# Optimization experiments

Measured on AMD Instinct MI355X. Metric: run time of the kernel, lower is better.

The kernel has to match this reference:

```python
import jax, jax.numpy as jnp
import numpy as np

DIM = 4096

def _fwht_unnormalized(y):
    # y: (T, d), iterative radix-2 butterfly, unnormalized Sylvester WHT
    d = y.shape[-1]
    h = 1
    while h < d:
        y = y.reshape(-1, d // (2 * h), 2, h)
        a = y[..., 0, :]
        b = y[..., 1, :]
        y = jnp.stack([a + b, a - b], axis=-2).reshape(-1, d)
        h *= 2
    return y

def setup_inputs() -> dict:
    key = jax.random.key(0)
    x = jax.random.normal(key, (4, 2048, DIM), dtype=jnp.float32)
    return {"x": x}

def reference(x):
    # Original: x_flat @ H.T where H is built recursively with a 1/sqrt(n)
    # division at EVERY recursion level. H is symmetric, and equals the
    # unnormalized Sylvester Hadamard times 2^{-L(L+1)/4}, L = log2(d).
    shape = x.shape
    d = shape[-1]
    L = int(round(np.log2(d)))
    scale = np.float32(2.0 ** (-(L * (L + 1)) / 4.0))
    y = _fwht_unnormalized(x.reshape(-1, d))
    return (y * scale).reshape(shape)
```

## Files before the change

kernel.cpp:

```cpp
#include <hip/hip_runtime.h>


constexpr int DIM = 4096;
constexpr int PITCH = 68;

__global__ __launch_bounds__(64) void fwht4096_kernel(const float* __restrict__ x,
                                                      float* __restrict__ y) {
    __shared__ float buf[64 * PITCH];
    const int lane = threadIdx.x;
    const long long row = blockIdx.x;

    float v[64];

    {
        const float4* src = reinterpret_cast<const float4*>(x + row * DIM + lane * 64);
#pragma unroll
        for (int q = 0; q < 16; ++q) {
            float4 t = src[q];
            v[4 * q + 0] = t.x;
            v[4 * q + 1] = t.y;
            v[4 * q + 2] = t.z;
            v[4 * q + 3] = t.w;
        }
    }

#pragma unroll
    for (int h = 1; h < 64; h <<= 1) {
#pragma unroll
        for (int i = 0; i < 64; i += 2 * h) {
#pragma unroll
            for (int k = 0; k < h; ++k) {
                float a = v[i + k];
                float b = v[i + k + h];
                v[i + k]     = a + b;
                v[i + k + h] = a - b;
            }
        }
    }

    {
        float* wp = buf + lane * PITCH;
#pragma unroll
        for (int q = 0; q < 16; ++q) {
            float4 t;
            t.x = v[4 * q + 0];
            t.y = v[4 * q + 1];
            t.z = v[4 * q + 2];
            t.w = v[4 * q + 3];
            reinterpret_cast<float4*>(wp)[q] = t;
        }
    }
    __syncthreads();

#pragma unroll
    for (int m = 0; m < 64; ++m) {
        v[m] = buf[m * PITCH + lane];
    }

#pragma unroll
    for (int h = 1; h < 64; h <<= 1) {
#pragma unroll
        for (int i = 0; i < 64; i += 2 * h) {
#pragma unroll
            for (int k = 0; k < h; ++k) {
                float a = v[i + k];
                float b = v[i + k + h];
                v[i + k]     = a + b;
                v[i + k + h] = a - b;
            }
        }
    }

    const float scale = 0x1p-39f;
    float* dst = y + row * DIM + lane;
#pragma unroll
    for (int m = 0; m < 64; ++m) {
        dst[m * 64] = v[m] * scale;
    }
}

extern "C" void kernel_launch(void* const* d_in, const int* in_sizes, int n_in,
                              void* d_out, int out_size, void* d_ws, size_t ws_size,
                              hipStream_t stream) {
    const float* x = (const float*)d_in[0];
    float* y = (float*)d_out;
    const int nrows = in_sizes[0] / DIM;
    fwht4096_kernel<<<nrows, 64, 0, stream>>>(x, y);
}
```

Measured before the change: 229.1 us.

## Split 4096-point FWHT into three radix-16 stages across 256 threads

Restructures the per-row transform from two radix-64 passes over 64 threads into three radix-16 passes over 256 threads, with two shared-memory transposes padded to 17 floats per row. Each thread now holds 16 values instead of 64, which cuts register pressure and raises occupancy and latency hiding for a memory-bound kernel. In exchange it adds an extra LDS round trip and more block barriers per row.

```diff
diff --git a/kernel.cpp b/kernel.cpp
--- a/kernel.cpp
+++ b/kernel.cpp
@@ -2,32 +2,12 @@
 
 
 constexpr int DIM = 4096;
-constexpr int PITCH = 68;
 
-__global__ __launch_bounds__(64) void fwht4096_kernel(const float* __restrict__ x,
-                                                      float* __restrict__ y) {
-    __shared__ float buf[64 * PITCH];
-    const int lane = threadIdx.x;
-    const long long row = blockIdx.x;
-
-    float v[64];
-
-    {
-        const float4* src = reinterpret_cast<const float4*>(x + row * DIM + lane * 64);
+__device__ __forceinline__ void fwht16(float v[16]) {
 #pragma unroll
-        for (int q = 0; q < 16; ++q) {
-            float4 t = src[q];
-            v[4 * q + 0] = t.x;
-            v[4 * q + 1] = t.y;
-            v[4 * q + 2] = t.z;
-            v[4 * q + 3] = t.w;
-        }
-    }
-
+    for (int h = 1; h < 16; h <<= 1) {
 #pragma unroll
-    for (int h = 1; h < 64; h <<= 1) {
-#pragma unroll
-        for (int i = 0; i < 64; i += 2 * h) {
+        for (int i = 0; i < 16; i += 2 * h) {
 #pragma unroll
             for (int k = 0; k < h; ++k) {
                 float a = v[i + k];
@@ -37,45 +17,67 @@
             }
         }
     }
+}
+
+__global__ __launch_bounds__(256, 8) void fwht4096_kernel(const float* __restrict__ x,
+                                                          float* __restrict__ y) {
+    __shared__ float buf[17 * 256];
+    const int t = threadIdx.x;
+    const long long row = blockIdx.x;
+    const int t_hi = t >> 4;
+    const int t_lo = t & 15;
+
+    float v[16];
 
     {
-        float* wp = buf + lane * PITCH;
+        const float4* src = reinterpret_cast<const float4*>(x + row * DIM + t * 16);
 #pragma unroll
-        for (int q = 0; q < 16; ++q) {
-            float4 t;
-            t.x = v[4 * q + 0];
-            t.y = v[4 * q + 1];
-            t.z = v[4 * q + 2];
-            t.w = v[4 * q + 3];
-            reinterpret_cast<float4*>(wp)[q] = t;
-        }
-    }
-    __syncthreads();
-
-#pragma unroll
-    for (int m = 0; m < 64; ++m) {
-        v[m] = buf[m * PITCH + lane];
-    }
-
-#pragma unroll
-    for (int h = 1; h < 64; h <<= 1) {
-#pragma unroll
-        for (int i = 0; i < 64; i += 2 * h) {
-#pragma unroll
-            for (int k = 0; k < h; ++k) {
-                float a = v[i + k];
-                float b = v[i + k + h];
-                v[i + k]     = a + b;
-                v[i + k + h] = a - b;
-            }
+        for (int q = 0; q < 4; ++q) {
+            float4 f = src[q];
+            v[4 * q + 0] = f.x;
+            v[4 * q + 1] = f.y;
+            v[4 * q + 2] = f.z;
+            v[4 * q + 3] = f.w;
         }
     }
 
+    fwht16(v);
+
+    {
+        float* wp = buf + 17 * t;
+#pragma unroll
+        for (int j = 0; j < 16; ++j) wp[j] = v[j];
+    }
+    __syncthreads();
+    {
+        const float* rp = buf + 272 * t_hi + t_lo;
+#pragma unroll
+        for (int j = 0; j < 16; ++j) v[j] = rp[17 * j];
+    }
+
+    fwht16(v);
+
+    __syncthreads();
+
+    {
+        float* wp = buf + 17 * t_lo + t_hi;
+#pragma unroll
+        for (int j = 0; j < 16; ++j) wp[272 * j] = v[j];
+    }
+    __syncthreads();
+    {
+        const float* rp = buf + 17 * t;
+#pragma unroll
+        for (int j = 0; j < 16; ++j) v[j] = rp[j];
+    }
+
+    fwht16(v);
+
     const float scale = 0x1p-39f;
-    float* dst = y + row * DIM + lane;
+    float* dst = y + row * DIM + t;
 #pragma unroll
-    for (int m = 0; m < 64; ++m) {
-        dst[m * 64] = v[m] * scale;
+    for (int j = 0; j < 16; ++j) {
+        dst[j * 256] = v[j] * scale;
     }
 }
 
@@ -85,5 +87,5 @@
     const float* x = (const float*)d_in[0];
     float* y = (float*)d_out;
     const int nrows = in_sizes[0] / DIM;
-    fwht4096_kernel<<<nrows, 64, 0, stream>>>(x, y);
+    fwht4096_kernel<<<nrows, 256, 0, stream>>>(x, y);
 }
```

Result: no change. 226.6 us (-1.1%).
